# Optimization experiments

Hardware: AMD Instinct MI355X
Metric: run time of the kernel (lower is better)

## Reference

```python
import jax, jax.numpy as jnp
import numpy as np

TEMPERATURE = 0.07
EPS = 1e-07


def setup_inputs() -> dict:
    key = jax.random.key(0)
    kf, kl = jax.random.split(key)
    bsz, n_views, d = 4096, 2, 256
    feats = jax.random.normal(kf, (bsz, n_views, d), dtype=jnp.float32)
    # L2-normalize per view, as in standard SupCon pipelines
    feats = feats / jnp.linalg.norm(feats, axis=-1, keepdims=True)
    labels = jax.random.randint(kl, (bsz,), 0, 3, dtype=jnp.int64 if jax.config.jax_enable_x64 else jnp.int32)
    return {"features": feats, "labels": labels}


def reference(features, labels):
    bsz, n_views, d = features.shape
    n = bsz * n_views
    # torch.cat(torch.unbind(features, dim=1), dim=0): views stacked along batch
    contrast_feature = jnp.transpose(features, (1, 0, 2)).reshape(n, d)
    anchor_feature = contrast_feature  # contrast_mode == 'all'

    # label-equality mask with the module's 1e-7 offset, tiled over views
    mask_small = (labels[:, None] == labels[None, :]).astype(jnp.float32) + EPS
    mask = jnp.tile(mask_small, (n_views, n_views))  # [n, n]

    logits_mask = 1.0 - jnp.eye(n, dtype=jnp.float32)  # zero out self-contrast
    mask_pos = mask * logits_mask
    mask_neg = (1.0 - mask) * logits_mask

    similarity = jnp.exp(jnp.matmul(anchor_feature, contrast_feature.T) / TEMPERATURE)
    pos = jnp.sum(similarity * mask_pos, axis=1)
    neg = jnp.sum(similarity * mask_neg, axis=1)
    loss = -jnp.mean(jnp.log(pos / (pos + neg)))
    return loss
```

## Files before the change

kernel.cpp:

```cpp
#include <hip/hip_runtime.h>
#include <cstdint>

#define BSZ   4096
#define NTOT  8192
#define DIM   256
#define BT    128
#define NCB   (NTOT / BT)
#define NBLK  (NCB * (NCB + 1) / 2)
#define INV_T16 (1.0f/(0.07f*16.0f))

typedef float f32x4 __attribute__((ext_vector_type(4)));

__device__ __forceinline__ unsigned short f2bf(float f) {
  unsigned int u = __float_as_uint(f);
  u = u + 0x7FFFu + ((u >> 16) & 1u);
  return (unsigned short)(u >> 16);
}

template <int CTRL>
__device__ __forceinline__ float dpp_radd(float v) {
  int r = __builtin_amdgcn_update_dpp(0, __float_as_int(v), CTRL, 0xF, 0xF, true);
  return v + __int_as_float(r);
}
__device__ __forceinline__ float row16_sum(float v) {
  v = dpp_radd<0x129>(v);
  v = dpp_radd<0x125>(v);
  v = dpp_radd<0x123>(v);
  v = dpp_radd<0x122>(v);
  return v;
}


__global__ __launch_bounds__(256) void cvt_kernel(const float* __restrict__ F,
                                                  unsigned char* __restrict__ Xf,
                                                  float* __restrict__ gsum,
                                                  int* __restrict__ gcnt) {
  __shared__ unsigned char lds[32 * 264];
  if (blockIdx.x == 0 && threadIdx.x == 0) { *gsum = 0.f; *gcnt = 0; }
  const int t  = threadIdx.x;
  const int R0 = blockIdx.x * 32;
#pragma unroll
  for (int k = 0; k < 8; ++k) {
    const int f   = t + k * 256;
    const int row = f >> 6;
    const int c4  = f & 63;
    const int r   = R0 + row;
    const float4 v = *(const float4*)(F + (size_t)(r & (BSZ - 1)) * (2 * DIM)
                                        + (r >> 12) * DIM + c4 * 4);
    int w = __builtin_amdgcn_cvt_pk_fp8_f32(v.x * 4.f, v.y * 4.f, 0, false);
    w     = __builtin_amdgcn_cvt_pk_fp8_f32(v.z * 4.f, v.w * 4.f, w, true);
    *(int*)(lds + row * 264 + c4 * 4) = w;
  }
  __syncthreads();
#pragma unroll
  for (int it = 0; it < 2; ++it) {
    const int o  = t + it * 256;
    const int Tl = o >> 8, m = (o >> 4) & 15, p = o & 15;
    const int P  = m >> 2, q = m & 3;
    const unsigned char* src = lds + (Tl * 16 + p) * 264 + P * 64 + q * 8;
    const uint2 lo = *(const uint2*)(src);
    const uint2 hi = *(const uint2*)(src + 32);
    *(uint4*)(Xf + (size_t)(blockIdx.x * 2 + Tl) * 4096 + m * 256 + p * 16) =
        make_uint4(lo.x, lo.y, hi.x, hi.y);
  }
}

__global__ __launch_bounds__(256, 3) void supcon_kernel(
    const unsigned char* __restrict__ Xf, const int* __restrict__ lab,
    float* __restrict__ partTot, float* __restrict__ partEq) {
  __shared__ float sbuf[1024];

  const int tid  = threadIdx.x;
  const int lane = tid & 63;
  const int wave = tid >> 6;
  const int wr   = (wave >> 1) * 64;
  const int wc   = (wave & 1) * 64;
  const int l15  = lane & 15;
  const int quad = lane >> 4;

  const int b = blockIdx.x;
  const int c = (b & 7) * (NBLK / 8) + (b >> 3);
  int i, j;
  if (c < 1792) {
    const int spo = c >> 6;
    const int w   = c & 63;
    int g1 = 0, rem = spo;
    while (rem >= 7 - g1) { rem -= 7 - g1; ++g1; }
    const int g2 = g1 + 1 + rem;
    i = g1 * 8 + (w >> 3);
    j = g2 * 8 + (w & 7);
  } else {
    const int c2 = c - 1792;
    const int g  = c2 / 36;
    int w = c2 - g * 36;
    int a = 0;
    while (w >= 8 - a) { w -= 8 - a; ++a; }
    i = g * 8 + a;
    j = g * 8 + a + w;
  }
  const int RB = i * BT;
  const int CB = j * BT;

  int colIdx[4], colLab[4];
#pragma unroll
  for (int tc = 0; tc < 4; ++tc) {
    colIdx[tc] = CB + wc + tc * 16 + l15;
    colLab[tc] = lab[colIdx[tc] & (BSZ - 1)];
  }
  int rowLab[4][4];
#pragma unroll
  for (int tr = 0; tr < 4; ++tr)
#pragma unroll
    for (int reg = 0; reg < 4; ++reg)
      rowLab[tr][reg] = lab[(RB + wr + tr * 16 + quad * 4 + reg) & (BSZ - 1)];

  const int TA = (RB >> 4) + (wave >> 1) * 4;
  const int TB = (CB >> 4) + (wave & 1) * 4;
  const int lo = quad * 256 + l15 * 16;

  f32x4 acc[4][4] = {};

#pragma unroll
  for (int P = 0; P < 4; ++P) {
    ulonglong2 aL[4], bL[4];
    const int ko = P * 1024 + lo;
#pragma unroll
    for (int t = 0; t < 4; ++t) {
      aL[t] = *(const ulonglong2*)(Xf + (size_t)(TA + t) * 4096 + ko);
      bL[t] = *(const ulonglong2*)(Xf + (size_t)(TB + t) * 4096 + ko);
    }
#pragma unroll
    for (int tr = 0; tr < 4; ++tr)
#pragma unroll
      for (int tc = 0; tc < 4; ++tc)
        acc[tr][tc] = __builtin_amdgcn_mfma_f32_16x16x32_fp8_fp8(
            (long)aL[tr].x, (long)bL[tc].x, acc[tr][tc], 0, 0, 0);
#pragma unroll
    for (int tr = 0; tr < 4; ++tr)
#pragma unroll
      for (int tc = 0; tc < 4; ++tc)
        acc[tr][tc] = __builtin_amdgcn_mfma_f32_16x16x32_fp8_fp8(
            (long)aL[tr].y, (long)bL[tc].y, acc[tr][tc], 0, 0, 0);
  }

  if (i == j) {
#pragma unroll
    for (int tr = 0; tr < 4; ++tr)
#pragma unroll
      for (int tc = 0; tc < 4; ++tc)
#pragma unroll
        for (int reg = 0; reg < 4; ++reg) {
          const int row = RB + wr + tr * 16 + quad * 4 + reg;
          float e = __expf(acc[tr][tc][reg] * INV_T16);
          acc[tr][tc][reg] = (colIdx[tc] == row) ? 0.f : e;
        }
  } else {
#pragma unroll
    for (int tr = 0; tr < 4; ++tr)
#pragma unroll
      for (int tc = 0; tc < 4; ++tc)
#pragma unroll
        for (int reg = 0; reg < 4; ++reg)
          acc[tr][tc][reg] = __expf(acc[tr][tc][reg] * INV_T16);
  }

#pragma unroll
  for (int tr = 0; tr < 4; ++tr) {
#pragma unroll
    for (int reg = 0; reg < 4; ++reg) {
      float tot = 0.f, eqs = 0.f;
#pragma unroll
      for (int tc = 0; tc < 4; ++tc) {
        const float e = acc[tr][tc][reg];
        tot += e;
        if (colLab[tc] == rowLab[tr][reg]) eqs += e;
      }
      tot = row16_sum(tot);
      eqs = row16_sum(eqs);
      if (l15 == 0) {
        const int rl_ = wr + tr * 16 + quad * 4 + reg;
        sbuf[(wave & 1) * 128 + rl_]       = tot;
        sbuf[256 + (wave & 1) * 128 + rl_] = eqs;
      }
    }
  }
  if (i != j) {
#pragma unroll
    for (int tc = 0; tc < 4; ++tc) {
      float tt = 0.f, te = 0.f;
#pragma unroll
      for (int tr = 0; tr < 4; ++tr)
#pragma unroll
        for (int reg = 0; reg < 4; ++reg) {
          const float e = acc[tr][tc][reg];
          tt += e;
          if (rowLab[tr][reg] == colLab[tc]) te += e;
        }
      tt += __shfl_xor(tt, 16, 64);  te += __shfl_xor(te, 16, 64);
      tt += __shfl_xor(tt, 32, 64);  te += __shfl_xor(te, 32, 64);
      if (quad == 0) {
        const int cl_ = wc + tc * 16 + l15;
        sbuf[512 + (wave >> 1) * 128 + cl_] = tt;
        sbuf[768 + (wave >> 1) * 128 + cl_] = te;
      }
    }
  }
  __syncthreads();

  if (tid < 128) {
    partTot[(size_t)j * NTOT + RB + tid] = sbuf[tid] + sbuf[128 + tid];
    partEq [(size_t)j * NTOT + RB + tid] = sbuf[256 + tid] + sbuf[384 + tid];
  } else if (i != j) {
    const int c2 = tid - 128;
    partTot[(size_t)i * NTOT + CB + c2] = sbuf[512 + c2] + sbuf[640 + c2];
    partEq [(size_t)i * NTOT + CB + c2] = sbuf[768 + c2] + sbuf[896 + c2];
  }
}

__global__ __launch_bounds__(128) void reduce_kernel(
    const float* __restrict__ partTot, const float* __restrict__ partEq,
    float* __restrict__ gsum, int* __restrict__ gcnt,
    unsigned int* __restrict__ out) {
  const int r = blockIdx.x * 128 + threadIdx.x;
  float tot = 0.f, eqs = 0.f;
#pragma unroll 8
  for (int cb = 0; cb < NCB; ++cb) {
    tot += partTot[(size_t)cb * NTOT + r];
    eqs += partEq [(size_t)cb * NTOT + r];
  }
  const float term = __logf((eqs + 1e-7f * tot) / tot);
  __shared__ float red[128];
  red[threadIdx.x] = term;
  __syncthreads();
  for (int step = 64; step > 0; step >>= 1) {
    if (threadIdx.x < step) red[threadIdx.x] += red[threadIdx.x + step];
    __syncthreads();
  }
  if (threadIdx.x == 0) {
    atomicAdd(gsum, red[0]);
    __threadfence();
    const int old = atomicAdd(gcnt, 1);
    if (old == (int)gridDim.x - 1) {
      __threadfence();
      const float total = atomicAdd(gsum, 0.0f);
      const float loss = -total / (float)NTOT;
      const unsigned short bb = f2bf(loss);
      out[0] = ((unsigned int)bb << 16) | (unsigned int)bb;
    }
  }
}

extern "C" void kernel_launch(void* const* d_in, const int* in_sizes, int n_in,
                              void* d_out, int out_size, void* d_ws, size_t ws_size,
                              hipStream_t stream) {
  (void)in_sizes; (void)n_in; (void)out_size; (void)ws_size;
  const float* feats = (const float*)d_in[0];
  const int*   labels = (const int*)d_in[1];

  char* ws = (char*)d_ws;
  unsigned char* Xf = (unsigned char*)ws;
  float* partTot = (float*)(ws + (size_t)NTOT * DIM);
  float* partEq  = partTot + (size_t)NCB * NTOT;
  float* gsum    = partEq  + (size_t)NCB * NTOT;
  int*   gcnt    = (int*)(gsum + 1);

  cvt_kernel<<<NTOT / 32, 256, 0, stream>>>(feats, Xf, gsum, gcnt);
  supcon_kernel<<<NBLK, 256, 0, stream>>>(Xf, labels, partTot, partEq);
  reduce_kernel<<<NTOT / 128, 128, 0, stream>>>(partTot, partEq, gsum, gcnt,
                                                (unsigned int*)d_out);
}
```

Measured before the change: 95.27 us.

## Switch FP8 GEMM to 32x32x64 scaled MFMA with matching operand layout

Replaces the 16x16x32 fp8 MFMA tiles with the gfx950 scaled 32x32x64 f8f6f4 MFMA, so each wave issues 4 larger MFMAs per K-step instead of 32 small ones. The conversion kernel is changed to write fp8 operands in a 32-row packed layout that this instruction consumes directly. The epilogue and row/column reduction are rewritten for the 32x32 accumulator layout, and row labels are now loaded per use as int4 vectors instead of being held in registers. This is meant to cut instruction-issue overhead and raise matrix-core throughput. The cost is heavier accumulator register pressure and cross-lane reductions that must match the new output layout exactly.

```diff
diff --git a/kernel.cpp b/kernel.cpp
--- a/kernel.cpp
+++ b/kernel.cpp
@@ -9,7 +9,8 @@
 #define NBLK  (NCB * (NCB + 1) / 2)
 #define INV_T16 (1.0f/(0.07f*16.0f))
 
-typedef float f32x4 __attribute__((ext_vector_type(4)));
+typedef float f32x16 __attribute__((ext_vector_type(16)));
+typedef int   i32x8  __attribute__((ext_vector_type(8)));
 
 __device__ __forceinline__ unsigned short f2bf(float f) {
   unsigned int u = __float_as_uint(f);
@@ -54,13 +55,15 @@
   __syncthreads();
 #pragma unroll
   for (int it = 0; it < 2; ++it) {
-    const int o  = t + it * 256;
-    const int Tl = o >> 8, m = (o >> 4) & 15, p = o & 15;
-    const int P  = m >> 2, q = m & 3;
-    const unsigned char* src = lds + (Tl * 16 + p) * 264 + P * 64 + q * 8;
+    const int o    = it * 256 + t;
+    const int P    = o >> 7;
+    const int part = (o >> 6) & 1;
+    const int l    = o & 63;
+    const int kh   = l >> 5, m = l & 31;
+    const unsigned char* src = lds + m * 264 + P * 64 + kh * 32 + part * 16;
     const uint2 lo = *(const uint2*)(src);
-    const uint2 hi = *(const uint2*)(src + 32);
-    *(uint4*)(Xf + (size_t)(blockIdx.x * 2 + Tl) * 4096 + m * 256 + p * 16) =
+    const uint2 hi = *(const uint2*)(src + 8);
+    *(uint4*)(Xf + (size_t)blockIdx.x * 8192 + P * 2048 + part * 1024 + l * 16) =
         make_uint4(lo.x, lo.y, hi.x, hi.y);
   }
 }
@@ -73,10 +76,8 @@
   const int tid  = threadIdx.x;
   const int lane = tid & 63;
   const int wave = tid >> 6;
-  const int wr   = (wave >> 1) * 64;
-  const int wc   = (wave & 1) * 64;
-  const int l15  = lane & 15;
-  const int quad = lane >> 4;
+  const int kh   = lane >> 5;
+  const int l31  = lane & 31;
 
   const int b = blockIdx.x;
   const int c = (b & 7) * (NBLK / 8) + (b >> 3);
@@ -101,108 +102,100 @@
   const int RB = i * BT;
   const int CB = j * BT;
 
-  int colIdx[4], colLab[4];
-#pragma unroll
-  for (int tc = 0; tc < 4; ++tc) {
-    colIdx[tc] = CB + wc + tc * 16 + l15;
+  int colIdx[2], colLab[2];
+#pragma unroll
+  for (int tc = 0; tc < 2; ++tc) {
+    colIdx[tc] = CB + (wave & 1) * 64 + tc * 32 + l31;
     colLab[tc] = lab[colIdx[tc] & (BSZ - 1)];
   }
-  int rowLab[4][4];
-#pragma unroll
-  for (int tr = 0; tr < 4; ++tr)
-#pragma unroll
-    for (int reg = 0; reg < 4; ++reg)
-      rowLab[tr][reg] = lab[(RB + wr + tr * 16 + quad * 4 + reg) & (BSZ - 1)];
-
-  const int TA = (RB >> 4) + (wave >> 1) * 4;
-  const int TB = (CB >> 4) + (wave & 1) * 4;
-  const int lo = quad * 256 + l15 * 16;
-
-  f32x4 acc[4][4] = {};
+
+  const size_t AT0 = (size_t)((RB >> 5) + (wave >> 1) * 2) * 8192;
+  const size_t BT0 = (size_t)((CB >> 5) + (wave & 1) * 2) * 8192;
+  const int lb = lane * 16;
+
+  f32x16 acc[2][2] = {};
 
 #pragma unroll
   for (int P = 0; P < 4; ++P) {
-    ulonglong2 aL[4], bL[4];
-    const int ko = P * 1024 + lo;
-#pragma unroll
-    for (int t = 0; t < 4; ++t) {
-      aL[t] = *(const ulonglong2*)(Xf + (size_t)(TA + t) * 4096 + ko);
-      bL[t] = *(const ulonglong2*)(Xf + (size_t)(TB + t) * 4096 + ko);
-    }
-#pragma unroll
-    for (int tr = 0; tr < 4; ++tr)
-#pragma unroll
-      for (int tc = 0; tc < 4; ++tc)
-        acc[tr][tc] = __builtin_amdgcn_mfma_f32_16x16x32_fp8_fp8(
-            (long)aL[tr].x, (long)bL[tc].x, acc[tr][tc], 0, 0, 0);
-#pragma unroll
-    for (int tr = 0; tr < 4; ++tr)
-#pragma unroll
-      for (int tc = 0; tc < 4; ++tc)
-        acc[tr][tc] = __builtin_amdgcn_mfma_f32_16x16x32_fp8_fp8(
-            (long)aL[tr].y, (long)bL[tc].y, acc[tr][tc], 0, 0, 0);
-  }
-
+    i32x8 a8[2], b8[2];
+#pragma unroll
+    for (int t = 0; t < 2; ++t) {
+      const unsigned char* pa = Xf + AT0 + t * 8192 + P * 2048 + lb;
+      const unsigned char* pb = Xf + BT0 + t * 8192 + P * 2048 + lb;
+      const uint4 alo = *(const uint4*)pa, ahi = *(const uint4*)(pa + 1024);
+      const uint4 blo = *(const uint4*)pb, bhi = *(const uint4*)(pb + 1024);
+      a8[t] = (i32x8){(int)alo.x, (int)alo.y, (int)alo.z, (int)alo.w,
+                      (int)ahi.x, (int)ahi.y, (int)ahi.z, (int)ahi.w};
+      b8[t] = (i32x8){(int)blo.x, (int)blo.y, (int)blo.z, (int)blo.w,
+                      (int)bhi.x, (int)bhi.y, (int)bhi.z, (int)bhi.w};
+    }
+#pragma unroll
+    for (int tr = 0; tr < 2; ++tr)
+#pragma unroll
+      for (int tc = 0; tc < 2; ++tc)
+        acc[tr][tc] = __builtin_amdgcn_mfma_scale_f32_32x32x64_f8f6f4(
+            a8[tr], b8[tc], acc[tr][tc], 0, 0,
+            0, 0x7F7F7F7F, 0, 0x7F7F7F7F);
+  }
+
+  const int rowB = RB + (wave >> 1) * 64 + 4 * kh;
   if (i == j) {
 #pragma unroll
-    for (int tr = 0; tr < 4; ++tr)
-#pragma unroll
-      for (int tc = 0; tc < 4; ++tc)
-#pragma unroll
-        for (int reg = 0; reg < 4; ++reg) {
-          const int row = RB + wr + tr * 16 + quad * 4 + reg;
-          float e = __expf(acc[tr][tc][reg] * INV_T16);
-          acc[tr][tc][reg] = (colIdx[tc] == row) ? 0.f : e;
+    for (int tr = 0; tr < 2; ++tr)
+#pragma unroll
+      for (int tc = 0; tc < 2; ++tc)
+#pragma unroll
+        for (int reg = 0; reg < 16; ++reg) {
+          const int row = rowB + tr * 32 + (reg & 3) + 8 * (reg >> 2);
+          const float e = __expf(acc[tr][tc][reg] * INV_T16);
+          acc[tr][tc][reg] = (row == colIdx[tc]) ? 0.f : e;
         }
   } else {
 #pragma unroll
-    for (int tr = 0; tr < 4; ++tr)
-#pragma unroll
-      for (int tc = 0; tc < 4; ++tc)
-#pragma unroll
-        for (int reg = 0; reg < 4; ++reg)
+    for (int tr = 0; tr < 2; ++tr)
+#pragma unroll
+      for (int tc = 0; tc < 2; ++tc)
+#pragma unroll
+        for (int reg = 0; reg < 16; ++reg)
           acc[tr][tc][reg] = __expf(acc[tr][tc][reg] * INV_T16);
   }
 
-#pragma unroll
-  for (int tr = 0; tr < 4; ++tr) {
-#pragma unroll
-    for (int reg = 0; reg < 4; ++reg) {
-      float tot = 0.f, eqs = 0.f;
-#pragma unroll
-      for (int tc = 0; tc < 4; ++tc) {
-        const float e = acc[tr][tc][reg];
-        tot += e;
-        if (colLab[tc] == rowLab[tr][reg]) eqs += e;
+  float bt0 = 0.f, bt1 = 0.f, be0 = 0.f, be1 = 0.f;
+#pragma unroll
+  for (int tr = 0; tr < 2; ++tr) {
+#pragma unroll
+    for (int rg = 0; rg < 4; ++rg) {
+      const int r0 = (rowB + tr * 32 + rg * 8) & (BSZ - 1);
+      const int4 L = *(const int4*)(lab + r0);
+      const int Ls[4] = {L.x, L.y, L.z, L.w};
+#pragma unroll
+      for (int rr = 0; rr < 4; ++rr) {
+        const int reg = rg * 4 + rr;
+        const int rl  = Ls[rr];
+        const float e0 = acc[tr][0][reg], e1 = acc[tr][1][reg];
+        const float s0 = (colLab[0] == rl) ? e0 : 0.f;
+        const float s1 = (colLab[1] == rl) ? e1 : 0.f;
+        bt0 += e0; bt1 += e1; be0 += s0; be1 += s1;
+        float tot = e0 + e1, eqs = s0 + s1;
+        tot = row16_sum(tot); tot += __shfl_xor(tot, 16, 64);
+        eqs = row16_sum(eqs); eqs += __shfl_xor(eqs, 16, 64);
+        if (l31 == 0) {
+          const int rib = (wave >> 1) * 64 + tr * 32 + rg * 8 + 4 * kh + rr;
+          sbuf[(wave & 1) * 128 + rib]       = tot;
+          sbuf[256 + (wave & 1) * 128 + rib] = eqs;
+        }
       }
-      tot = row16_sum(tot);
-      eqs = row16_sum(eqs);
-      if (l15 == 0) {
-        const int rl_ = wr + tr * 16 + quad * 4 + reg;
-        sbuf[(wave & 1) * 128 + rl_]       = tot;
-        sbuf[256 + (wave & 1) * 128 + rl_] = eqs;
-      }
     }
   }
   if (i != j) {
-#pragma unroll
-    for (int tc = 0; tc < 4; ++tc) {
-      float tt = 0.f, te = 0.f;
-#pragma unroll
-      for (int tr = 0; tr < 4; ++tr)
-#pragma unroll
-        for (int reg = 0; reg < 4; ++reg) {
-          const float e = acc[tr][tc][reg];
-          tt += e;
-          if (rowLab[tr][reg] == colLab[tc]) te += e;
-        }
-      tt += __shfl_xor(tt, 16, 64);  te += __shfl_xor(te, 16, 64);
-      tt += __shfl_xor(tt, 32, 64);  te += __shfl_xor(te, 32, 64);
-      if (quad == 0) {
-        const int cl_ = wc + tc * 16 + l15;
-        sbuf[512 + (wave >> 1) * 128 + cl_] = tt;
-        sbuf[768 + (wave >> 1) * 128 + cl_] = te;
-      }
+    bt0 += __shfl_xor(bt0, 32, 64);  be0 += __shfl_xor(be0, 32, 64);
+    bt1 += __shfl_xor(bt1, 32, 64);  be1 += __shfl_xor(be1, 32, 64);
+    if (lane < 32) {
+      const int cib = (wave & 1) * 64 + l31;
+      sbuf[512 + (wave >> 1) * 128 + cib]      = bt0;
+      sbuf[512 + (wave >> 1) * 128 + cib + 32] = bt1;
+      sbuf[768 + (wave >> 1) * 128 + cib]      = be0;
+      sbuf[768 + (wave >> 1) * 128 + cib + 32] = be1;
     }
   }
   __syncthreads();
```

After: 98.35 us. 1.03x slower.
